# Kernel optimization log

Hardware: AMD Instinct MI355X
Metric: run time of the kernel (lower is better)

## Reference

```python
import jax, jax.numpy as jnp
import numpy as np

N_NODES = 50000
N_EDGES = 800000
D_IN = 256
D_HID = 256
N_CLASSES = 40


def gcn_conv(x, W, b, src, dst, deg_inv_sqrt, n):
    # PyG GCNConv: linear transform first, then normalized scatter-add aggregation.
    x = x @ W                                   # [N, d_out]
    norm = deg_inv_sqrt[src] * deg_inv_sqrt[dst]  # [E+N] sym norm with self-loops
    msgs = x[src] * norm[:, None]               # gather source features
    out = jax.ops.segment_sum(msgs, dst, num_segments=n)
    return out + b


def setup_inputs() -> dict:
    key = jax.random.key(0)
    ks = jax.random.split(key, 6)
    x = jax.random.normal(ks[0], (N_NODES, D_IN), dtype=jnp.float32)
    edge_index = jax.random.randint(ks[1], (2, N_EDGES), 0, N_NODES, dtype=jnp.int64)
    s_in = 1.0 / np.sqrt(D_IN)
    s_h = 1.0 / np.sqrt(D_HID)
    W0 = jax.random.normal(ks[2], (D_IN, D_HID), dtype=jnp.float32) * s_in
    b0 = jnp.zeros((D_HID,), dtype=jnp.float32)
    W1 = jax.random.normal(ks[3], (D_HID, D_HID), dtype=jnp.float32) * s_h
    b1 = jnp.zeros((D_HID,), dtype=jnp.float32)
    W2 = jax.random.normal(ks[4], (D_HID, N_CLASSES), dtype=jnp.float32) * s_h
    b2 = jnp.zeros((N_CLASSES,), dtype=jnp.float32)
    return {"x": x, "edge_index": edge_index, "W0": W0, "b0": b0,
            "W1": W1, "b1": b1, "W2": W2, "b2": b2}


def reference(x, edge_index, W0, b0, W1, b1, W2, b2):
    n = x.shape[0]
    loops = jnp.arange(n, dtype=edge_index.dtype)
    src = jnp.concatenate([edge_index[0], loops])
    dst = jnp.concatenate([edge_index[1], loops])
    # degree (with self-loops) on destination nodes; deg >= 1 so rsqrt is safe
    deg = jax.ops.segment_sum(jnp.ones_like(dst, dtype=x.dtype), dst, num_segments=n)
    deg_inv_sqrt = jax.lax.rsqrt(deg)

    h = gcn_conv(x, W0, b0, src, dst, deg_inv_sqrt, n)
    h = jax.nn.relu(h)  # dropout is identity in eval mode
    h = gcn_conv(h, W1, b1, src, dst, deg_inv_sqrt, n)
    h = jax.nn.relu(h)
    h = gcn_conv(h, W2, b2, src, dst, deg_inv_sqrt, n)
    return jax.nn.log_softmax(h, axis=1)
```

## Files before the change

### kernel.cpp

```cpp
#include <hip/hip_runtime.h>
#include <hip/hip_bf16.h>
#include <cstdint>
#include <cstddef>


typedef unsigned char u8;
typedef unsigned short u16;
typedef unsigned int u32;
typedef __attribute__((ext_vector_type(8))) short bf16x8;
typedef __attribute__((ext_vector_type(4))) float f32x4;
typedef __attribute__((ext_vector_type(2))) float f32x2;

__device__ inline u16 f2bf(float f) {
  __hip_bfloat16 h = __float2bfloat16(f);
  return __builtin_bit_cast(u16, h);
}
__device__ inline u32 pk2bf(float lo, float hi) {
  return ((u32)f2bf(hi) << 16) | (u32)f2bf(lo);
}
__device__ inline u32 pk4fp8(float a, float b, float c, float d) {
  u32 w = __builtin_amdgcn_cvt_pk_fp8_f32(a, b, 0, false);
  w = __builtin_amdgcn_cvt_pk_fp8_f32(c, d, w, true);
  return w;
}
__device__ inline void up4fp8(u32 w, float* a) {
  f32x2 lo = __builtin_amdgcn_cvt_pk_f32_fp8(w, false);
  f32x2 hi = __builtin_amdgcn_cvt_pk_f32_fp8(w, true);
  a[0] += lo[0]; a[1] += lo[1]; a[2] += hi[0]; a[3] += hi[1];
}

__device__ inline void gl_lds16(const u16* g, u16* ldsbase) {
  __builtin_amdgcn_global_load_lds(
      (const __attribute__((address_space(1))) u32*)g,
      (__attribute__((address_space(3))) u32*)ldsbase, 16, 0, 0);
}

__global__ void k_prepcvtcount(const float* __restrict__ W0,
                               const float* __restrict__ W1,
                               const float* __restrict__ W2,
                               u16* __restrict__ Wt0, u16* __restrict__ Wt1,
                               u16* __restrict__ Wt2, int* __restrict__ bflag,
                               u8* __restrict__ zu8, u8* __restrict__ z40,
                               const float* __restrict__ x, u16* __restrict__ xb,
                               int total8,
                               const int* __restrict__ dst, int* __restrict__ cnt,
                               int* __restrict__ rank, int E,
                               int PB, int VB, int n) {
  const int bid = blockIdx.x;
  if (bid < PB) {
    const int t = bid * 256 + threadIdx.x;
    if (t < 65536) {
      const int k = t >> 8, c = t & 255;
      Wt0[c * 256 + k] = f2bf(W0[t]);
      Wt1[c * 256 + k] = f2bf(W1[t]);
    } else if (t < 65536 + 16384) {
      const int t2 = t - 65536;
      const int k = t2 >> 6, nn = t2 & 63;
      const float v = (nn < 40) ? W2[k * 40 + nn] : 0.f;
      Wt2[nn * 256 + k] = f2bf(v);
    } else {
      const int u = t - (65536 + 16384);
      if (u < 64) bflag[u] = 0;
      if (u < 256) zu8[u] = 0;
      if (u < 40) z40[u] = 0;
    }
    return;
  }
  if (bid < PB + VB) {
    const int i = (bid - PB) * 256 + threadIdx.x;
    if (i < total8) {
      const float4 lo = ((const float4*)x)[2 * i];
      const float4 hi = ((const float4*)x)[2 * i + 1];
      uint4 w;
      w.x = pk2bf(lo.x, lo.y); w.y = pk2bf(lo.z, lo.w);
      w.z = pk2bf(hi.x, hi.y); w.w = pk2bf(hi.z, hi.w);
      ((uint4*)xb)[i] = w;
    }
    return;
  }
  const int e = (bid - PB - VB) * 256 + threadIdx.x;
  if (e < E) rank[e] = atomicAdd(&cnt[dst[e]], 1);
}

__global__ __launch_bounds__(1024) void k_scan(const int* __restrict__ cnt,
                                               int* __restrict__ rs,
                                               float* __restrict__ dis,
                                               int* __restrict__ bval,
                                               int* __restrict__ bpre,
                                               int* __restrict__ bflag, int n) {
  __shared__ int wsum[16];
  __shared__ int sbase;
  const int b = blockIdx.x;
  const int tid = threadIdx.x;
  const int lane = tid & 63, wid = tid >> 6;
  const int i = b * 1024 + tid;
  const int v = (i < n) ? cnt[i] : 0;
  int x = v;
#pragma unroll
  for (int off = 1; off < 64; off <<= 1) {
    int y = __shfl_up(x, off, 64);
    if (lane >= off) x += y;
  }
  if (lane == 63) wsum[wid] = x;
  __syncthreads();
  if (wid == 0) {
    int w = (lane < 16) ? wsum[lane] : 0;
#pragma unroll
    for (int off = 1; off < 16; off <<= 1) {
      int y = __shfl_up(w, off, 64);
      if (lane >= off) w += y;
    }
    if (lane < 16) wsum[lane] = w;
  }
  __syncthreads();
  const int total = wsum[15];
  const int excl = (wid > 0 ? wsum[wid - 1] : 0) + (x - v);

  if (tid == 0) {
    if (b == 0) {
      atomicExch(&bpre[0], total);
      __threadfence();
      atomicExch(&bflag[0], 2);
      sbase = 0;
    } else {
      atomicExch(&bval[b], total);
      __threadfence();
      atomicExch(&bflag[b], 1);
      int run = 0, j = b - 1;
      while (true) {
        int f;
        while ((f = atomicAdd(&bflag[j], 0)) == 0) {}
        if (f == 2) { run += atomicAdd(&bpre[j], 0); break; }
        run += atomicAdd(&bval[j], 0);
        --j;
      }
      atomicExch(&bpre[b], run + total);
      __threadfence();
      atomicExch(&bflag[b], 2);
      sbase = run;
    }
  }
  __syncthreads();
  const int base = sbase;
  if (i < n) {
    rs[i] = base + excl;
    dis[i] = rsqrtf((float)(1 + v));
  }
  if (b == (int)gridDim.x - 1 && tid == 0) rs[n] = base + total;
}

__device__ inline void gemm256_body(const u16* __restrict__ A,
                                    const u16* __restrict__ Wt,
                                    const float* __restrict__ dis,
                                    u8* __restrict__ C, int M,
                                    int bx, int by, u16* As, u16* Bs) {
  const int tid = threadIdx.x;
  const int wid = tid >> 6, lane = tid & 63;
  const int wave_m = wid >> 1, wave_n = wid & 1;
  const int m0 = bx * 128, n0 = by * 128;
  const int quad = lane >> 4, col = lane & 15;

  const int srl = lane >> 3;
  const int sseg = lane & 7;

  const int ra = wave_m * 64 + col;
  const int rb = wave_n * 64 + col;

  f32x4 acc[4][4];
#pragma unroll
  for (int i = 0; i < 4; ++i)
#pragma unroll
    for (int j = 0; j < 4; ++j) acc[i][j] = (f32x4){0.f, 0.f, 0.f, 0.f};

  for (int k0 = 0; k0 < 256; k0 += 64) {
#pragma unroll
    for (int blk = 0; blk < 4; ++blk) {
      const int R = wid * 32 + blk * 8;
      const int r = R + srl;
      const int q = (sseg - r) & 7;
      if (m0 + r < M)
        gl_lds16(A + (size_t)(m0 + r) * 256 + k0 + q * 8, &As[R * 64]);
      gl_lds16(Wt + (size_t)(n0 + r) * 256 + k0 + q * 8, &Bs[R * 64]);
    }
    __syncthreads();

#pragma unroll
    for (int kk = 0; kk < 2; ++kk) {
      bf16x8 af[4], bf[4];
#pragma unroll
      for (int i = 0; i < 4; ++i) {
        const int r = ra + i * 16;
        af[i] = *(const bf16x8*)&As[r * 64 + ((quad + kk * 4 + r) & 7) * 8];
      }
#pragma unroll
      for (int j = 0; j < 4; ++j) {
        const int r = rb + j * 16;
        bf[j] = *(const bf16x8*)&Bs[r * 64 + ((quad + kk * 4 + r) & 7) * 8];
      }
#pragma unroll
      for (int i = 0; i < 4; ++i)
#pragma unroll
        for (int j = 0; j < 4; ++j)
          acc[i][j] = __builtin_amdgcn_mfma_f32_16x16x32_bf16(bf[j], af[i], acc[i][j], 0, 0, 0);
    }
    __syncthreads();
  }

#pragma unroll
  for (int i = 0; i < 4; ++i) {
    const int m = m0 + wave_m * 64 + i * 16 + col;
    if (m < M) {
      const float dd = dis[m];
#pragma unroll
      for (int j = 0; j < 4; ++j) {
        const int n = n0 + wave_n * 64 + j * 16 + quad * 4;
        const u32 w = pk4fp8(acc[i][j][0] * dd, acc[i][j][1] * dd,
                             acc[i][j][2] * dd, acc[i][j][3] * dd);
        *(u32*)(C + (size_t)m * 256 + n) = w;
      }
    }
  }
}

__global__ __launch_bounds__(256) void k_gemmfill(
    const u16* __restrict__ xb, const u16* __restrict__ Wt0,
    const float* __restrict__ dis, u8* __restrict__ C, int M,
    const int* __restrict__ src, const int* __restrict__ dst,
    const int* __restrict__ rank, const int* __restrict__ rs,
    int* __restrict__ csr, int E, int GB) {
  __shared__ u16 As[128 * 64];
  __shared__ u16 Bs[128 * 64];
  if ((int)blockIdx.x >= GB) {
    const int e = (blockIdx.x - GB) * 256 + threadIdx.x;
    if (e < E) csr[rs[dst[e]] + rank[e]] = src[e];
    return;
  }
  gemm256_body(xb, Wt0, dis, C, M, blockIdx.x >> 1, blockIdx.x & 1, As, Bs);
}

__global__ __launch_bounds__(256) void k_gemm256(const u16* __restrict__ A,
                                                 const u16* __restrict__ Wt,
                                                 const float* __restrict__ dis,
                                                 u8* __restrict__ C, int M) {
  __shared__ u16 As[128 * 64];
  __shared__ u16 Bs[128 * 64];
  gemm256_body(A, Wt, dis, C, M, blockIdx.x, blockIdx.y, As, Bs);
}

__global__ __launch_bounds__(256) void k_agg256(const u8* __restrict__ u,
                                                const int* __restrict__ rs,
                                                const int* __restrict__ csr,
                                                const float* __restrict__ dis,
                                                const float* __restrict__ b,
                                                u16* __restrict__ out, int n) {
  const int wid = threadIdx.x >> 6, lane = threadIdx.x & 63;
  const int d = blockIdx.x * 4 + wid;
  if (d >= n) return;
  const int q = lane >> 4, sl = lane & 15;
  const int cb = sl * 16;
  float a[16] = {0.f, 0.f, 0.f, 0.f, 0.f, 0.f, 0.f, 0.f,
                 0.f, 0.f, 0.f, 0.f, 0.f, 0.f, 0.f, 0.f};
  {
    const int sidx = q ? n : d;
    const uint4 v = *(const uint4*)(u + (size_t)sidx * 256 + cb);
    up4fp8(v.x, a); up4fp8(v.y, a + 4); up4fp8(v.z, a + 8); up4fp8(v.w, a + 12);
  }
  const int p1 = rs[d + 1];
  for (int p = rs[d]; p < p1; p += 16) {
    int idx[4];
#pragma unroll
    for (int i = 0; i < 4; ++i) {
      const int e = p + 4 * i + q;
      idx[i] = (e < p1) ? csr[e] : n;
    }
    uint4 v[4];
#pragma unroll
    for (int i = 0; i < 4; ++i)
      v[i] = *(const uint4*)(u + (size_t)idx[i] * 256 + cb);
#pragma unroll
    for (int i = 0; i < 4; ++i) {
      up4fp8(v[i].x, a); up4fp8(v[i].y, a + 4);
      up4fp8(v[i].z, a + 8); up4fp8(v[i].w, a + 12);
    }
  }
#pragma unroll
  for (int j = 0; j < 16; ++j) {
    a[j] += __shfl_xor(a[j], 16, 64);
    a[j] += __shfl_xor(a[j], 32, 64);
  }
  if (q == 0) {
    const float dd = dis[d];
    uint4 o0, o1;
    const float4 b0 = *(const float4*)(b + cb);
    const float4 b1 = *(const float4*)(b + cb + 4);
    const float4 b2 = *(const float4*)(b + cb + 8);
    const float4 b3 = *(const float4*)(b + cb + 12);
    o0.x = pk2bf(fmaxf(dd * a[0] + b0.x, 0.f), fmaxf(dd * a[1] + b0.y, 0.f));
    o0.y = pk2bf(fmaxf(dd * a[2] + b0.z, 0.f), fmaxf(dd * a[3] + b0.w, 0.f));
    o0.z = pk2bf(fmaxf(dd * a[4] + b1.x, 0.f), fmaxf(dd * a[5] + b1.y, 0.f));
    o0.w = pk2bf(fmaxf(dd * a[6] + b1.z, 0.f), fmaxf(dd * a[7] + b1.w, 0.f));
    o1.x = pk2bf(fmaxf(dd * a[8] + b2.x, 0.f), fmaxf(dd * a[9] + b2.y, 0.f));
    o1.y = pk2bf(fmaxf(dd * a[10] + b2.z, 0.f), fmaxf(dd * a[11] + b2.w, 0.f));
    o1.z = pk2bf(fmaxf(dd * a[12] + b3.x, 0.f), fmaxf(dd * a[13] + b3.y, 0.f));
    o1.w = pk2bf(fmaxf(dd * a[14] + b3.z, 0.f), fmaxf(dd * a[15] + b3.w, 0.f));
    *(uint4*)(out + (size_t)d * 256 + cb) = o0;
    *(uint4*)(out + (size_t)d * 256 + cb + 8) = o1;
  }
}

__global__ __launch_bounds__(256) void k_gemm40(const u16* __restrict__ A,
                                                const u16* __restrict__ Wt2,
                                                const float* __restrict__ dis,
                                                u8* __restrict__ C, int M) {
  const int wv = threadIdx.x >> 6, lane = threadIdx.x & 63;
  const int quad = lane >> 4, col = lane & 15;
  const int m0 = blockIdx.x * 128 + wv * 32;
  f32x4 acc[2][3];
#pragma unroll
  for (int i = 0; i < 2; ++i)
#pragma unroll
    for (int j = 0; j < 3; ++j) acc[i][j] = (f32x4){0.f, 0.f, 0.f, 0.f};
  for (int k0 = 0; k0 < 256; k0 += 32) {
    bf16x8 af[2], bf[3];
#pragma unroll
    for (int i = 0; i < 2; ++i) {
      int row = m0 + i * 16 + col;
      row = (row < M) ? row : (M - 1);
      af[i] = *(const bf16x8*)(A + (size_t)row * 256 + k0 + quad * 8);
    }
#pragma unroll
    for (int j = 0; j < 3; ++j)
      bf[j] = *(const bf16x8*)(Wt2 + (size_t)(j * 16 + col) * 256 + k0 + quad * 8);
#pragma unroll
    for (int i = 0; i < 2; ++i)
#pragma unroll
      for (int j = 0; j < 3; ++j)
        acc[i][j] = __builtin_amdgcn_mfma_f32_16x16x32_bf16(bf[j], af[i], acc[i][j], 0, 0, 0);
  }
#pragma unroll
  for (int i = 0; i < 2; ++i) {
    const int m = m0 + i * 16 + col;
    if (m < M) {
      const float dd = dis[m];
#pragma unroll
      for (int j = 0; j < 3; ++j) {
        const int nn = j * 16 + quad * 4;
        if (nn < 40) {
          const u32 w = pk4fp8(acc[i][j][0] * dd, acc[i][j][1] * dd,
                               acc[i][j][2] * dd, acc[i][j][3] * dd);
          *(u32*)(C + (size_t)m * 40 + nn) = w;
        }
      }
    }
  }
}

__global__ __launch_bounds__(256) void k_agg40(const u8* __restrict__ u,
                                               const int* __restrict__ rs,
                                               const int* __restrict__ csr,
                                               const float* __restrict__ dis,
                                               const float* __restrict__ b,
                                               float* __restrict__ out, int n) {
  const int wid = threadIdx.x >> 6, lane = threadIdx.x & 63;
  const int d = blockIdx.x * 4 + wid;
  if (d >= n) return;
  const int slot = lane / 10;
  const int sl = lane % 10;
  const bool act = slot < 6;
  float a[4] = {0.f, 0.f, 0.f, 0.f};
  if (slot == 0) {
    const u32 v = *(const u32*)(u + (size_t)d * 40 + sl * 4);
    up4fp8(v, a);
  }
  const int p1 = rs[d + 1];
  for (int p = rs[d]; p < p1; p += 24) {
    int idx[4];
#pragma unroll
    for (int i = 0; i < 4; ++i) {
      const int e = p + 6 * i + slot;
      idx[i] = (act && e < p1) ? csr[e] : n;
    }
    u32 v[4];
#pragma unroll
    for (int i = 0; i < 4; ++i)
      v[i] = *(const u32*)(u + (size_t)idx[i] * 40 + sl * 4);
#pragma unroll
    for (int i = 0; i < 4; ++i) up4fp8(v[i], a);
  }
#pragma unroll
  for (int k = 0; k < 4; ++k) {
    const float t = __shfl(a[k], lane + 30, 64);
    a[k] += t;
  }
#pragma unroll
  for (int k = 0; k < 4; ++k) {
    const float t1 = __shfl(a[k], lane + 10, 64);
    const float t2 = __shfl(a[k], lane + 20, 64);
    a[k] += t1 + t2;
  }
  float l[4];
  float mx = -INFINITY;
  const bool head = lane < 10;
  if (head) {
    const float dd = dis[d];
#pragma unroll
    for (int k = 0; k < 4; ++k) {
      l[k] = dd * a[k] + b[lane * 4 + k];
      mx = fmaxf(mx, l[k]);
    }
  }
#pragma unroll
  for (int off = 8; off; off >>= 1) mx = fmaxf(mx, __shfl_xor(mx, off, 64));
  float sm = 0.f;
  if (head) {
#pragma unroll
    for (int k = 0; k < 4; ++k) sm += expf(l[k] - mx);
  }
#pragma unroll
  for (int off = 8; off; off >>= 1) sm += __shfl_xor(sm, off, 64);
  if (head) {
    const float ls = mx + logf(sm);
    float4 o = make_float4(l[0] - ls, l[1] - ls, l[2] - ls, l[3] - ls);
    *(float4*)(out + (size_t)d * 40 + lane * 4) = o;
  }
}

extern "C" void kernel_launch(void* const* d_in, const int* in_sizes, int n_in,
                              void* d_out, int out_size, void* d_ws, size_t ws_size,
                              hipStream_t stream) {
  const float* x  = (const float*)d_in[0];
  const int*   ei = (const int*)d_in[1];
  const float* W0 = (const float*)d_in[2];
  const float* b0 = (const float*)d_in[3];
  const float* W1 = (const float*)d_in[4];
  const float* b1 = (const float*)d_in[5];
  const float* W2 = (const float*)d_in[6];
  const float* b2 = (const float*)d_in[7];
  float* out = (float*)d_out;

  const int N = in_sizes[0] / 256;
  const int E = in_sizes[1] / 2;
  const int* src = ei;
  const int* dst = ei + E;

  char* p = (char*)d_ws;
  auto carve = [&](size_t bytes) {
    char* q = p;
    p += (bytes + 255) & ~(size_t)255;
    return q;
  };
  u16*   xb    = (u16*)carve((size_t)N * 256 * 2);
  u8*    uf8   = (u8*)carve((size_t)(N + 1) * 256);
  u16*   h     = (u16*)carve((size_t)N * 256 * 2);
  u8*    u40   = (u8*)carve((size_t)(N + 1) * 40);
  u16*   Wt0   = (u16*)carve(256 * 256 * 2);
  u16*   Wt1   = (u16*)carve(256 * 256 * 2);
  u16*   Wt2   = (u16*)carve(64 * 256 * 2);
  float* dis   = (float*)carve((size_t)N * 4);
  int*   cnt   = (int*)carve((size_t)N * 4);
  int*   rs    = (int*)carve((size_t)(N + 1) * 4);
  int*   rank  = (int*)carve((size_t)E * 4);
  int*   csr   = (int*)carve((size_t)(E + 32) * 4);
  int*   bval  = (int*)carve(64 * 4);
  int*   bpre  = (int*)carve(64 * 4);
  int*   bflag = (int*)carve(64 * 4);

  const int PB = (65536 + 16384 + 256 + 255) / 256;
  const int total8 = N * 256 / 8;
  const int VB = (total8 + 255) / 256;
  const int CB = (E + 255) / 256;
  const int GB = ((N + 127) / 128) * 2;
  const int nb = (N + 1023) / 1024;
  const int agrid = (N + 3) / 4;

  hipMemsetAsync(cnt, 0, (size_t)N * 4, stream);

  k_prepcvtcount<<<PB + VB + CB, 256, 0, stream>>>(
      W0, W1, W2, Wt0, Wt1, Wt2, bflag,
      uf8 + (size_t)N * 256, u40 + (size_t)N * 40,
      x, xb, total8, dst, cnt, rank, E, PB, VB, N);
  k_scan<<<nb, 1024, 0, stream>>>(cnt, rs, dis, bval, bpre, bflag, N);
  k_gemmfill<<<GB + CB, 256, 0, stream>>>(xb, Wt0, dis, uf8, N,
                                          src, dst, rank, rs, csr, E, GB);
  k_agg256<<<agrid, 256, 0, stream>>>(uf8, rs, csr, dis, b0, h, N);
  k_gemm256<<<dim3((N + 127) / 128, 2), 256, 0, stream>>>(h, Wt1, dis, uf8, N);
  k_agg256<<<agrid, 256, 0, stream>>>(uf8, rs, csr, dis, b1, h, N);
  k_gemm40<<<(N + 127) / 128, 256, 0, stream>>>(h, Wt2, dis, u40, N);
  k_agg40<<<agrid, 256, 0, stream>>>(u40, rs, csr, dis, b2, out, N);
}
```

Baseline: 306.3 us.

## Overlap degree counting with first GEMM by moving source scaling into aggregation

The first GEMM no longer needs the degree-based source scale, so it now runs alongside the edge-count atomics before the scan. The per-source dis scale moves into the first aggregation, which gathers dis[src] for each edge. The CSR fill becomes its own kernel after the scan, and the cnt memset is folded into the prep kernel. The cost is an extra kernel launch and extra per-edge dis loads and multiplies in layer-1 aggregation. Storing unscaled values in fp8 also changes rounding slightly.

```diff
diff --git a/kernel.cpp b/kernel.cpp
--- a/kernel.cpp
+++ b/kernel.cpp
@@ -23,10 +23,10 @@
   w = __builtin_amdgcn_cvt_pk_fp8_f32(c, d, w, true);
   return w;
 }
-__device__ inline void up4fp8(u32 w, float* a) {
+__device__ inline void up4fp8(u32 w, float* a, float s) {
   f32x2 lo = __builtin_amdgcn_cvt_pk_f32_fp8(w, false);
   f32x2 hi = __builtin_amdgcn_cvt_pk_f32_fp8(w, true);
-  a[0] += lo[0]; a[1] += lo[1]; a[2] += hi[0]; a[3] += hi[1];
+  a[0] += s * lo[0]; a[1] += s * lo[1]; a[2] += s * hi[0]; a[3] += s * hi[1];
 }
 
 __device__ inline void gl_lds16(const u16* g, u16* ldsbase) {
@@ -35,17 +35,15 @@
       (__attribute__((address_space(3))) u32*)ldsbase, 16, 0, 0);
 }
 
-__global__ void k_prepcvtcount(const float* __restrict__ W0,
-                               const float* __restrict__ W1,
-                               const float* __restrict__ W2,
-                               u16* __restrict__ Wt0, u16* __restrict__ Wt1,
-                               u16* __restrict__ Wt2, int* __restrict__ bflag,
-                               u8* __restrict__ zu8, u8* __restrict__ z40,
-                               const float* __restrict__ x, u16* __restrict__ xb,
-                               int total8,
-                               const int* __restrict__ dst, int* __restrict__ cnt,
-                               int* __restrict__ rank, int E,
-                               int PB, int VB, int n) {
+__global__ void k_prepcvt(const float* __restrict__ W0,
+                          const float* __restrict__ W1,
+                          const float* __restrict__ W2,
+                          u16* __restrict__ Wt0, u16* __restrict__ Wt1,
+                          u16* __restrict__ Wt2, int* __restrict__ bflag,
+                          int* __restrict__ cnt,
+                          u8* __restrict__ zu8, u8* __restrict__ z40,
+                          const float* __restrict__ x, u16* __restrict__ xb,
+                          int total8, int PB, int n) {
   const int bid = blockIdx.x;
   if (bid < PB) {
     const int t = bid * 256 + threadIdx.x;
@@ -60,26 +58,22 @@
       Wt2[nn * 256 + k] = f2bf(v);
     } else {
       const int u = t - (65536 + 16384);
+      if (u < n) cnt[u] = 0;
       if (u < 64) bflag[u] = 0;
       if (u < 256) zu8[u] = 0;
       if (u < 40) z40[u] = 0;
     }
     return;
   }
-  if (bid < PB + VB) {
-    const int i = (bid - PB) * 256 + threadIdx.x;
-    if (i < total8) {
-      const float4 lo = ((const float4*)x)[2 * i];
-      const float4 hi = ((const float4*)x)[2 * i + 1];
-      uint4 w;
-      w.x = pk2bf(lo.x, lo.y); w.y = pk2bf(lo.z, lo.w);
-      w.z = pk2bf(hi.x, hi.y); w.w = pk2bf(hi.z, hi.w);
-      ((uint4*)xb)[i] = w;
-    }
-    return;
-  }
-  const int e = (bid - PB - VB) * 256 + threadIdx.x;
-  if (e < E) rank[e] = atomicAdd(&cnt[dst[e]], 1);
+  const int i = (bid - PB) * 256 + threadIdx.x;
+  if (i < total8) {
+    const float4 lo = ((const float4*)x)[2 * i];
+    const float4 hi = ((const float4*)x)[2 * i + 1];
+    uint4 w;
+    w.x = pk2bf(lo.x, lo.y); w.y = pk2bf(lo.z, lo.w);
+    w.z = pk2bf(hi.x, hi.y); w.w = pk2bf(hi.z, hi.w);
+    ((uint4*)xb)[i] = w;
+  }
 }
 
 __global__ __launch_bounds__(1024) void k_scan(const int* __restrict__ cnt,
@@ -149,6 +143,7 @@
   if (b == (int)gridDim.x - 1 && tid == 0) rs[n] = base + total;
 }
 
+template <bool SCALED>
 __device__ inline void gemm256_body(const u16* __restrict__ A,
                                     const u16* __restrict__ Wt,
                                     const float* __restrict__ dis,
@@ -210,7 +205,7 @@
   for (int i = 0; i < 4; ++i) {
     const int m = m0 + wave_m * 64 + i * 16 + col;
     if (m < M) {
-      const float dd = dis[m];
+      const float dd = SCALED ? dis[m] : 1.0f;
 #pragma unroll
       for (int j = 0; j < 4; ++j) {
         const int n = n0 + wave_n * 64 + j * 16 + quad * 4;
@@ -222,20 +217,27 @@
   }
 }
 
-__global__ __launch_bounds__(256) void k_gemmfill(
+__global__ __launch_bounds__(256) void k_gemmcount(
     const u16* __restrict__ xb, const u16* __restrict__ Wt0,
-    const float* __restrict__ dis, u8* __restrict__ C, int M,
-    const int* __restrict__ src, const int* __restrict__ dst,
-    const int* __restrict__ rank, const int* __restrict__ rs,
-    int* __restrict__ csr, int E, int GB) {
+    u8* __restrict__ C, int M,
+    const int* __restrict__ dst, int* __restrict__ cnt,
+    int* __restrict__ rank, int E, int GB) {
   __shared__ u16 As[128 * 64];
   __shared__ u16 Bs[128 * 64];
   if ((int)blockIdx.x >= GB) {
     const int e = (blockIdx.x - GB) * 256 + threadIdx.x;
-    if (e < E) csr[rs[dst[e]] + rank[e]] = src[e];
+    if (e < E) rank[e] = atomicAdd(&cnt[dst[e]], 1);
     return;
   }
-  gemm256_body(xb, Wt0, dis, C, M, blockIdx.x >> 1, blockIdx.x & 1, As, Bs);
+  gemm256_body<false>(xb, Wt0, nullptr, C, M, blockIdx.x >> 1, blockIdx.x & 1,
+                      As, Bs);
+}
+
+__global__ void k_fill(const int* __restrict__ src, const int* __restrict__ dst,
+                       const int* __restrict__ rank, const int* __restrict__ rs,
+                       int* __restrict__ csr, int E) {
+  int e = blockIdx.x * blockDim.x + threadIdx.x;
+  if (e < E) csr[rs[dst[e]] + rank[e]] = src[e];
 }
 
 __global__ __launch_bounds__(256) void k_gemm256(const u16* __restrict__ A,
@@ -244,9 +246,10 @@
                                                  u8* __restrict__ C, int M) {
   __shared__ u16 As[128 * 64];
   __shared__ u16 Bs[128 * 64];
-  gemm256_body(A, Wt, dis, C, M, blockIdx.x, blockIdx.y, As, Bs);
-}
-
+  gemm256_body<true>(A, Wt, dis, C, M, blockIdx.x, blockIdx.y, As, Bs);
+}
+
+template <bool SRCSCALE>
 __global__ __launch_bounds__(256) void k_agg256(const u8* __restrict__ u,
                                                 const int* __restrict__ rs,
                                                 const int* __restrict__ csr,
@@ -262,8 +265,10 @@
                  0.f, 0.f, 0.f, 0.f, 0.f, 0.f, 0.f, 0.f};
   {
     const int sidx = q ? n : d;
+    const float s = SRCSCALE ? (q ? 0.f : dis[d]) : 1.f;
     const uint4 v = *(const uint4*)(u + (size_t)sidx * 256 + cb);
-    up4fp8(v.x, a); up4fp8(v.y, a + 4); up4fp8(v.z, a + 8); up4fp8(v.w, a + 12);
+    up4fp8(v.x, a, s); up4fp8(v.y, a + 4, s);
+    up4fp8(v.z, a + 8, s); up4fp8(v.w, a + 12, s);
   }
   const int p1 = rs[d + 1];
   for (int p = rs[d]; p < p1; p += 16) {
@@ -274,13 +279,16 @@
       idx[i] = (e < p1) ? csr[e] : n;
     }
     uint4 v[4];
-#pragma unroll
-    for (int i = 0; i < 4; ++i)
+    float s[4];
+#pragma unroll
+    for (int i = 0; i < 4; ++i) {
       v[i] = *(const uint4*)(u + (size_t)idx[i] * 256 + cb);
+      s[i] = SRCSCALE ? ((idx[i] < n) ? dis[idx[i]] : 0.f) : 1.f;
+    }
 #pragma unroll
     for (int i = 0; i < 4; ++i) {
-      up4fp8(v[i].x, a); up4fp8(v[i].y, a + 4);
-      up4fp8(v[i].z, a + 8); up4fp8(v[i].w, a + 12);
+      up4fp8(v[i].x, a, s[i]); up4fp8(v[i].y, a + 4, s[i]);
+      up4fp8(v[i].z, a + 8, s[i]); up4fp8(v[i].w, a + 12, s[i]);
     }
   }
 #pragma unroll
@@ -370,7 +378,7 @@
   float a[4] = {0.f, 0.f, 0.f, 0.f};
   if (slot == 0) {
     const u32 v = *(const u32*)(u + (size_t)d * 40 + sl * 4);
-    up4fp8(v, a);
+    up4fp8(v, a, 1.f);
   }
   const int p1 = rs[d + 1];
   for (int p = rs[d]; p < p1; p += 24) {
@@ -385,7 +393,7 @@
     for (int i = 0; i < 4; ++i)
       v[i] = *(const u32*)(u + (size_t)idx[i] * 40 + sl * 4);
 #pragma unroll
-    for (int i = 0; i < 4; ++i) up4fp8(v[i], a);
+    for (int i = 0; i < 4; ++i) up4fp8(v[i], a, 1.f);
   }
 #pragma unroll
   for (int k = 0; k < 4; ++k) {
@@ -465,7 +473,7 @@
   int*   bpre  = (int*)carve(64 * 4);
   int*   bflag = (int*)carve(64 * 4);
 
-  const int PB = (65536 + 16384 + 256 + 255) / 256;
+  const int PB = (65536 + 16384 + N + 255) / 256;
   const int total8 = N * 256 / 8;
   const int VB = (total8 + 255) / 256;
   const int CB = (E + 255) / 256;
@@ -473,18 +481,17 @@
   const int nb = (N + 1023) / 1024;
   const int agrid = (N + 3) / 4;
 
-  hipMemsetAsync(cnt, 0, (size_t)N * 4, stream);
-
-  k_prepcvtcount<<<PB + VB + CB, 256, 0, stream>>>(
-      W0, W1, W2, Wt0, Wt1, Wt2, bflag,
-      uf8 + (size_t)N * 256, u40 + (size_t)N * 40,
-      x, xb, total8, dst, cnt, rank, E, PB, VB, N);
+  k_prepcvt<<<PB + VB, 256, 0, stream>>>(W0, W1, W2, Wt0, Wt1, Wt2, bflag, cnt,
+                                         uf8 + (size_t)N * 256,
+                                         u40 + (size_t)N * 40,
+                                         x, xb, total8, PB, N);
+  k_gemmcount<<<GB + CB, 256, 0, stream>>>(xb, Wt0, uf8, N,
+                                           dst, cnt, rank, E, GB);
   k_scan<<<nb, 1024, 0, stream>>>(cnt, rs, dis, bval, bpre, bflag, N);
-  k_gemmfill<<<GB + CB, 256, 0, stream>>>(xb, Wt0, dis, uf8, N,
-                                          src, dst, rank, rs, csr, E, GB);
-  k_agg256<<<agrid, 256, 0, stream>>>(uf8, rs, csr, dis, b0, h, N);
+  k_fill<<<CB, 256, 0, stream>>>(src, dst, rank, rs, csr, E);
+  k_agg256<true><<<agrid, 256, 0, stream>>>(uf8, rs, csr, dis, b0, h, N);
   k_gemm256<<<dim3((N + 127) / 128, 2), 256, 0, stream>>>(h, Wt1, dis, uf8, N);
-  k_agg256<<<agrid, 256, 0, stream>>>(uf8, rs, csr, dis, b1, h, N);
+  k_agg256<false><<<agrid, 256, 0, stream>>>(uf8, rs, csr, dis, b1, h, N);
   k_gemm40<<<(N + 127) / 128, 256, 0, stream>>>(h, Wt2, dis, u40, N);
   k_agg40<<<agrid, 256, 0, stream>>>(u40, rs, csr, dis, b2, out, N);
 }
```

New measurement: 310.9 us. About the same (+1.5%).
